# Kernel tuning notes

Measured on AMD Instinct MI355X. Metric: run time of the kernel, lower is better.

Reference implementation:

```python
import jax, jax.numpy as jnp
import numpy as np

B, C, H, W = 8, 256, 96, 96
NQ, NCLS = 100, 12
OBJ_CH = NCLS - 2 + 1  # 11
EPS = 1e-6


def conv2d(x, w, b, pad):
    out = jax.lax.conv_general_dilated(x, w, (1, 1), [(pad, pad), (pad, pad)],
                                       dimension_numbers=('NCHW', 'OIHW', 'NCHW'))
    return out + b[None, :, None, None]


def conv1d(x, w, b):
    out = jax.lax.conv_general_dilated(x, w, (1,), [(0, 0)],
                                       dimension_numbers=('NCH', 'OIH', 'NCH'))
    return out + b[None, :, None]


def adaptive_avg_pool_1d(x, out_size):
    # x: [..., L]; torch AdaptiveAvgPool semantics: bin i = mean(x[floor(i*L/o):ceil((i+1)*L/o)])
    L = x.shape[-1]
    i = np.arange(out_size)
    starts = (i * L) // out_size
    ends = -((-(i + 1) * L) // out_size)
    csum = jnp.concatenate([jnp.zeros(x.shape[:-1] + (1,), x.dtype), jnp.cumsum(x, -1)], -1)
    sizes = jnp.asarray((ends - starts).astype(np.float32))
    return (csum[..., ends] - csum[..., starts]) / sizes


def local_max(p):
    # 8-neighbor local maximum with zero padding, thresholded at EPS
    pd = jnp.pad(p, ((0, 0), (0, 0), (1, 1), (1, 1)))
    m = ((p >= pd[:, :, :-2, 1:-1]) & (p >= pd[:, :, 2:, 1:-1]) &
         (p >= pd[:, :, 1:-1, :-2]) & (p >= pd[:, :, 1:-1, 2:]) &
         (p >= pd[:, :, :-2, :-2]) & (p >= pd[:, :, :-2, 2:]) &
         (p >= pd[:, :, 2:, :-2]) & (p >= pd[:, :, 2:, 2:]) & (p >= EPS))
    return m.astype(p.dtype)


def mask_and_nms(probs):
    # one-hot mask from argmax over foreground channels, then add local-max map
    oh = jax.nn.one_hot(jnp.argmax(probs[:, :-1], axis=1), probs.shape[1], axis=1, dtype=probs.dtype)
    p = probs * oh
    return p + local_max(p)


def head(x, w1, b1, w2, b2):
    return conv2d(jax.nn.relu(conv2d(x, w1, b1, 1)), w2, b2, 0)


def setup_inputs() -> dict:
    key = jax.random.key(0)
    ks = jax.random.split(key, 20)
    rn = lambda k, s: jax.random.normal(k, s, jnp.float32) * 0.02
    z = lambda n: jnp.zeros((n,), jnp.float32)
    return {
        'x': jax.random.normal(ks[0], (B, C, H, W), jnp.float32),
        'y': jax.random.normal(ks[1], (B, C, H, W), jnp.float32),
        'pos_embeddings': jax.random.normal(ks[2], (1, C, H, W), jnp.float32),
        'lw1': rn(ks[3], (C, C, 3, 3)), 'lb1': z(C),
        'lw2': rn(ks[4], (2, C, 1, 1)), 'lb2': z(2),
        'rw1': rn(ks[5], (C, C, 3, 3)), 'rb1': z(C),
        'rw2': rn(ks[6], (2, C, 1, 1)), 'rb2': z(2),
        'ow1': rn(ks[7], (C, C, 3, 3)), 'ob1': z(C),
        'ow2': rn(ks[8], (OBJ_CH, C, 1, 1)), 'ob2': z(OBJ_CH),
        'cw1': rn(ks[9], (64, C, 3, 3)), 'cb1': z(64),
        'cw2': rn(ks[10], (32, 64, 3, 3)), 'cb2': z(32),
        'cm_lw': rn(ks[11], (778 * 2, 778 * 32)), 'cm_lb': z(778 * 2),
        'c1d_w': rn(ks[12], (C, 2, 3)), 'c1d_b': z(C),
        'q_lw': rn(ks[13], (NQ * C, C)), 'q_lb': z(NQ * C),
    }


def reference(x, y, pos_embeddings, lw1, lb1, lw2, lb2, rw1, rb1, rw2, rb2,
              ow1, ob1, ow2, ob2, cw1, cb1, cw2, cb2, cm_lw, cm_lb,
              c1d_w, c1d_b, q_lw, q_lb):
    b = x.shape[0]
    left_logits = head(x, lw1, lb1, lw2, lb2)
    right_logits = head(x, rw1, rb1, rw2, rb2)
    obj_logits = head(x, ow1, ob1, ow2, ob2)

    left_p = mask_and_nms(jax.nn.softmax(left_logits, axis=1))
    right_p = mask_and_nms(jax.nn.softmax(right_logits, axis=1))
    obj_p = mask_and_nms(jax.nn.softmax(obj_logits, axis=1))

    hw = H * W
    idx_l = jax.lax.top_k(left_p[:, 0].reshape(b, hw), 40)[1]
    idx_r = jax.lax.top_k(right_p[:, 0].reshape(b, hw), 40)[1]
    idx_o = jax.lax.top_k(obj_p[:, :-1].reshape(b, OBJ_CH - 1, hw).max(axis=1), 20)[1]
    idx = jnp.concatenate([idx_l, idx_r, idx_o], axis=1)  # [B, 100]

    xf = x.reshape(b, C, hw)
    topk_proposals = jnp.take_along_axis(xf, jnp.broadcast_to(idx[:, None, :], (b, C, NQ)), axis=2)
    pf = jnp.broadcast_to(pos_embeddings, (b, C, H, W)).reshape(b, C, hw)
    topk_pos = jnp.take_along_axis(pf, jnp.broadcast_to(idx[:, None, :], (b, C, NQ)), axis=2)

    # contact map estimation branch
    h = jax.nn.relu(conv2d(y, cw1, cb1, 1))
    h = jax.nn.relu(conv2d(h, cw2, cb2, 1))  # [B,32,H,W]
    h = jnp.mean(h, axis=3)                  # adaptive pool width -> 1
    h = adaptive_avg_pool_1d(h, 778)         # [B,32,778]
    cm = h.reshape(b, -1) @ cm_lw.T + cm_lb  # [B,1556]
    contact_map = cm.reshape(b, 2, 778, 1)

    # ContactMapConvolution
    cc = conv1d(contact_map.reshape(b, 2, 778), c1d_w, c1d_b)  # [B,C,776]
    cc = jnp.mean(cc, axis=2)                                  # [B,C]
    feat = (cc @ q_lw.T + q_lb).reshape(b, C, NQ)              # [B,C,100]

    topk_proposals = topk_proposals + feat
    return (topk_proposals, topk_pos, left_logits, right_logits, obj_logits, contact_map)
```

## Files before the change

kernel.cpp:

```cpp
#include <hip/hip_runtime.h>
#include <float.h>
#include <math.h>

#define B_ 8
#define C_ 256
#define H_ 96
#define W_ 96
#define HW_ 9216
#define NQ_ 100
#define EPS_ 1e-6f
#define PADW_ 98
#define PADIMG_ 9604
#define PALLOC_ 76880

typedef unsigned short ushort_t;
typedef __attribute__((ext_vector_type(8))) short bf16x8;
typedef __attribute__((ext_vector_type(16))) float f32x16;

typedef __attribute__((address_space(3))) unsigned int as3_u32;
typedef __attribute__((address_space(1))) unsigned int as1_u32;

__device__ __forceinline__ void gl16(const void* g, void* l) {
    __builtin_amdgcn_global_load_lds(
        (const as1_u32*)(unsigned long long)g,
        (as3_u32*)(unsigned int)(unsigned long long)l, 16, 0, 0);
}

__device__ __forceinline__ ushort_t bf16_of(float v) {
    unsigned u = __float_as_uint(v);
    u += 0x7fffu + ((u >> 16) & 1u);
    return (ushort_t)(u >> 16);
}
__device__ __forceinline__ float f_of_bf16(ushort_t h) {
    return __uint_as_float((unsigned)h << 16);
}

__global__ __launch_bounds__(256)
void zero_border_kernel(ushort_t* __restrict__ bh, ushort_t* __restrict__ bl, int Cch)
{
    int per = 388 * Cch / 8;
    int id = blockIdx.x * 256 + threadIdx.x;
    if (id >= 8 * per) return;
    int b = id / per, i = id - b * per;
    int pi = (i * 8) / Cch, c8 = (i * 8) % Cch;
    int yy, xx;
    if (pi < 98)      { yy = 0;            xx = pi; }
    else if (pi < 196){ yy = 97;           xx = pi - 98; }
    else if (pi < 292){ yy = pi - 195;     xx = 0; }
    else              { yy = pi - 291;     xx = 97; }
    size_t base = ((size_t)b * PADIMG_ + yy * PADW_ + xx) * Cch + c8;
    *(bf16x8*)&bh[base] = (bf16x8)(short)0;
    *(bf16x8*)&bl[base] = (bf16x8)(short)0;
}

__global__ __launch_bounds__(256)
void tsplit_kernel(const float* __restrict__ in, ushort_t* __restrict__ oh,
                   ushort_t* __restrict__ ol, int Cch)
{
    __shared__ float T[32][33];
    const int tx = threadIdx.x & 31, ty = threadIdx.x >> 5;
    const int p0 = blockIdx.x * 32, ci0 = blockIdx.y * 32, b = blockIdx.z;
#pragma unroll
    for (int i = 0; i < 4; ++i)
        T[ty + 8*i][tx] = in[((size_t)b*Cch + ci0 + ty + 8*i)*HW_ + p0 + tx];
    __syncthreads();
    const int y = p0 / 96, x0 = p0 - y * 96;
    const size_t Pp = (size_t)b*PADIMG_ + (size_t)(y + 1)*PADW_ + x0 + 1;
#pragma unroll
    for (int i = 0; i < 4; ++i) {
        float v = T[tx][ty + 8*i];
        ushort_t hi = bf16_of(v);
        float lo = v - f_of_bf16(hi);
        size_t o = (Pp + ty + 8*i)*Cch + ci0 + tx;
        oh[o] = hi;
        ol[o] = bf16_of(lo);
    }
}

__global__ __launch_bounds__(256)
void repack_kernel(const float* __restrict__ w, ushort_t* __restrict__ wh,
                   ushort_t* __restrict__ wl, int Cout, int Cin)
{
    int id = blockIdx.x*256 + threadIdx.x;
    int tot = 9*Cout*Cin;
    if (id >= tot) return;
    int tap = id / (Cout*Cin);
    int r   = id - tap*(Cout*Cin);
    int g   = r / (Cout*16);
    int r2  = r - g*(Cout*16);
    int oc  = r2 >> 4, cr = r2 & 15;
    int ci  = g*16 + cr;
    float v = w[((size_t)oc*Cin + ci)*9 + tap];
    ushort_t hi = bf16_of(v);
    wh[id] = hi;
    wl[id] = bf16_of(v - f_of_bf16(hi));
}

__global__ __launch_bounds__(256)
void pack_heads3_kernel(const float* lb1, const float* rb1, const float* ob1,
                        const float* lw2, const float* rw2, const float* ow2,
                        const float* lb2, const float* rb2, const float* ob2,
                        float* __restrict__ bias1all, float* __restrict__ w2all,
                        float* __restrict__ b2all)
{
    int i = blockIdx.x * 256 + threadIdx.x;
    if (i < 768) bias1all[i] = (i < 256) ? lb1[i] : (i < 512) ? rb1[i-256] : ob1[i-512];
    if (i < 33) {
        int h = i / 11, k = i - h*11;
        b2all[i] = (h == 0) ? (k < 2 ? lb2[k] : 0.f)
                 : (h == 1) ? (k < 2 ? rb2[k] : 0.f)
                 : ob2[k];
    }
    if (i < 3*11*256) {
        int h = i / 2816, r = i - h*2816;
        int k = r / 256, oc = r - k*256;
        float v = 0.f;
        if (h == 0)      { if (k < 2) v = lw2[k*256 + oc]; }
        else if (h == 1) { if (k < 2) v = rw2[k*256 + oc]; }
        else             v = ow2[k*256 + oc];
        w2all[i] = v;
    }
}

template<int WM, int WN, int MFR, int NFR, int CIN, int MODE>
__global__ __launch_bounds__(WM*WN*64, (WM*WN + 3) / 4)
void conv_gemm_kernel(const ushort_t* __restrict__ Agh, const ushort_t* __restrict__ Agl,
                      const ushort_t* __restrict__ Wgh, const ushort_t* __restrict__ Wgl,
                      const float* __restrict__ bias1,
                      ushort_t* __restrict__ Oth, ushort_t* __restrict__ Otl,
                      float* __restrict__ outf)
{
    constexpr int NW    = WM*WN;
    constexpr int NT    = NW*64;
    constexpr int BM    = WM*MFR*32;
    constexpr int COUT  = WN*NFR*32;
    constexpr int NG    = CIN/16;
    constexpr int APAD  = 512;
    constexpr int ASZ   = 2*APAD*16;
    constexpr int AROUNDS = 32;
    static_assert(BM == 288, "BM must be 288");

    __shared__ __align__(16) ushort_t ALds[2*ASZ];

    const int tid  = threadIdx.x;
    const int lane = tid & 63;
    const int wid  = __builtin_amdgcn_readfirstlane(tid >> 6);
    const int wm   = wid / WN, wn = wid % WN;
    const int l31  = lane & 31, hh2 = lane >> 5;
    const int wnb  = wn * NFR * 32;

    const int cpx = gridDim.x >> 3;
    const int bid = (blockIdx.x & 7)*cpx + (blockIdx.x >> 3);
    const int bidx = bid >> 5;
    const int br   = bid & 31;
    const size_t S = (size_t)bidx*PADIMG_ + (size_t)(3*br)*PADW_;

    auto stageA = [&](int g, int sel) {
        ushort_t* dst = ALds + sel*ASZ;
#pragma unroll 1
        for (int c = wid; c < AROUNDS; c += NW) {
            int id = c*64 + lane;
            int split = id >> 10;
            int r2 = id & 1023;
            int row = r2 >> 1, slot = r2 & 1;
            int ch = slot ^ ((row >> 2) & 1);
            const ushort_t* src = (split ? Agl : Agh) + (S + row)*CIN + g*16 + ch*8;
            gl16(src, dst + (size_t)c*512);
        }
    };

    f32x16 acc[MFR][NFR];
#pragma unroll
    for (int i = 0; i < MFR; ++i)
#pragma unroll
        for (int j = 0; j < NFR; ++j)
#pragma unroll
            for (int r = 0; r < 16; ++r) acc[i][j][r] = 0.f;

    bf16x8 bh0[NFR], bl0[NFR], bh1[NFR], bl1[NFR], bh2[NFR], bl2[NFR];

#define LOADB(G, T, BH, BL)                                                    \
    {                                                                          \
        _Pragma("unroll")                                                      \
        for (int nf = 0; nf < NFR; ++nf) {                                     \
            size_t o = ((size_t)((T)*NG + (G))*COUT + (wnb + nf*32 + l31))*16  \
                       + hh2*8;                                                \
            BH[nf] = *(const bf16x8*)&Wgh[o];                                  \
            BL[nf] = *(const bf16x8*)&Wgl[o];                                  \
        }                                                                      \
    }

    stageA(0, 0);
    LOADB(0, 0, bh0, bl0);
    LOADB(0, 1, bh1, bl1);
    __builtin_amdgcn_sched_barrier(0);
    asm volatile("s_waitcnt vmcnt(%0)" :: "n"(4*NFR) : "memory");
    __builtin_amdgcn_s_barrier();
    __builtin_amdgcn_sched_barrier(0);

#define TAPBODY(T, BHC, BLC, BHN, BLN)                                         \
    {                                                                          \
        if ((T) <= 6)            LOADB(g,     (T)+2, BHN, BLN)                 \
        else if (g + 1 < NG)     LOADB(g+1,   (T)-7, BHN, BLN)                 \
        const int tapoff = ((T)/3)*PADW_ + ((T) % 3);                          \
        _Pragma("unroll")                                                      \
        for (int mf = 0; mf < MFR; ++mf) {                                     \
            int row = wm*PADW_ + tapoff + mf*32 + l31;                         \
            int o = abase + row*16 + ((hh2 ^ ((row >> 2) & 1)) << 3);          \
            bf16x8 ah = *(const bf16x8*)&ALds[o];                              \
            bf16x8 al = *(const bf16x8*)&ALds[o + APAD*16];                    \
            _Pragma("unroll")                                                  \
            for (int nf = 0; nf < NFR; ++nf) {                                 \
                acc[mf][nf] = __builtin_amdgcn_mfma_f32_32x32x16_bf16(         \
                    ah, BHC[nf], acc[mf][nf], 0, 0, 0);                        \
                acc[mf][nf] = __builtin_amdgcn_mfma_f32_32x32x16_bf16(         \
                    al, BHC[nf], acc[mf][nf], 0, 0, 0);                        \
                acc[mf][nf] = __builtin_amdgcn_mfma_f32_32x32x16_bf16(         \
                    ah, BLC[nf], acc[mf][nf], 0, 0, 0);                        \
            }                                                                  \
        }                                                                      \
    }

#pragma unroll 1
    for (int g = 0; g < NG; ++g) {
        if (g + 1 < NG) stageA(g + 1, (g + 1) & 1);
        const int abase = (g & 1) * ASZ;
        TAPBODY(0, bh0, bl0, bh2, bl2);
        TAPBODY(1, bh1, bl1, bh0, bl0);
        TAPBODY(2, bh2, bl2, bh1, bl1);
        TAPBODY(3, bh0, bl0, bh2, bl2);
        TAPBODY(4, bh1, bl1, bh0, bl0);
        TAPBODY(5, bh2, bl2, bh1, bl1);
        TAPBODY(6, bh0, bl0, bh2, bl2);
        TAPBODY(7, bh1, bl1, bh0, bl0);
        TAPBODY(8, bh2, bl2, bh1, bl1);
        __builtin_amdgcn_sched_barrier(0);
        asm volatile("s_waitcnt lgkmcnt(0)" ::: "memory");
        asm volatile("s_waitcnt vmcnt(%0)" :: "n"(4*NFR) : "memory");
        __builtin_amdgcn_s_barrier();
        __builtin_amdgcn_sched_barrier(0);
    }
#undef TAPBODY
#undef LOADB
    __syncthreads();

    float biasv[NFR];
#pragma unroll
    for (int nf = 0; nf < NFR; ++nf) biasv[nf] = bias1[wnb + nf*32 + l31];

    if constexpr (MODE == 1) {
#pragma unroll
        for (int mf = 0; mf < MFR; ++mf)
#pragma unroll
            for (int nf = 0; nf < NFR; ++nf)
#pragma unroll
                for (int r = 0; r < 16; ++r) {
                    float rr = fmaxf(acc[mf][nf][r] + biasv[nf], 0.f);
                    ushort_t hi = bf16_of(rr);
                    float lo = rr - f_of_bf16(hi);
                    int crow = (r & 3) + 8*(r >> 2) + 4*hh2;
                    int xx = mf*32 + crow;
                    size_t Pp = (size_t)bidx*PADIMG_
                              + (size_t)(3*br + wm + 1)*PADW_ + xx + 1;
                    size_t o = Pp*COUT + wnb + nf*32 + l31;
                    Oth[o] = hi;
                    Otl[o] = bf16_of(lo);
                }
    } else {
        float (*T)[BM + 1] = (float(*)[BM + 1])ALds;
#pragma unroll
        for (int mf = 0; mf < MFR; ++mf)
#pragma unroll
            for (int r = 0; r < 16; ++r) {
                float rr = fmaxf(acc[mf][0][r] + biasv[0], 0.f);
                int crow = (r & 3) + 8*(r >> 2) + 4*hh2;
                T[l31][wm*96 + mf*32 + crow] = rr;
            }
        __syncthreads();
        for (int i = tid; i < COUT*BM; i += NT) {
            int c = i / BM, m = i - c*BM;
            outf[((size_t)bidx*COUT + c)*HW_ + br*288 + m] = T[c][m];
        }
    }
}

__global__ __launch_bounds__(256, 3)
void conv_sbu_kernel(const ushort_t* __restrict__ Agh, const ushort_t* __restrict__ Agl,
                     const ushort_t* __restrict__ wLh, const ushort_t* __restrict__ wLl,
                     const ushort_t* __restrict__ wRh, const ushort_t* __restrict__ wRl,
                     const ushort_t* __restrict__ wOh, const ushort_t* __restrict__ wOl,
                     const float* __restrict__ bias1all, const float* __restrict__ w2all,
                     const float* __restrict__ b2all, float* __restrict__ out_logits)
{
    constexpr int NG = 16, APAD = 304, ASZ = 2*APAD*16, AGR = 19, MFR = 3, NFR = 2;
    __shared__ __align__(16) ushort_t ALds[ASZ];

    const int tid  = threadIdx.x;
    const int lane = tid & 63;
    const int wid  = __builtin_amdgcn_readfirstlane(tid >> 6);
    const int l31  = lane & 31, hh2 = lane >> 5;
    const int wnb  = wid * 64;

    const int cpx = gridDim.x >> 3;
    const int bid = (blockIdx.x & 7)*cpx + (blockIdx.x >> 3);
    const int h    = bid / 768;
    const int sub  = bid - h*768;
    const int bidx = sub / 96, prow = sub - bidx*96;
    const int pimg0 = prow * 96;
    const size_t S = (size_t)bidx*PADIMG_ + (size_t)prow*PADW_;

    const ushort_t* Wh = (h == 0) ? wLh : (h == 1) ? wRh : wOh;
    const ushort_t* Wl = (h == 0) ? wLl : (h == 1) ? wRl : wOl;
    const float* bias1 = bias1all + h*256;
    const float* w2    = w2all + (size_t)h*2816;
    const float* b2    = b2all + h*11;
    const int kklim = (h == 2) ? 11 : 2;
    float* dst = out_logits + ((h == 0) ? 0 : (h == 1) ? 147456 : 294912);

    auto stageA = [&](int g) {
#pragma unroll 1
        for (int c = wid; c < AGR; c += 4) {
            int id = c*64 + lane;
            int split = id / (2*APAD);
            int r2 = id % (2*APAD);
            int row = r2 >> 1, slot = r2 & 1;
            int ch = slot ^ ((row >> 2) & 1);
            const ushort_t* src = (split ? Agl : Agh) + (S + row)*C_ + g*16 + ch*8;
            gl16(src, ALds + (size_t)c*512);
        }
    };

    f32x16 acc[MFR][NFR];
#pragma unroll
    for (int i = 0; i < MFR; ++i)
#pragma unroll
        for (int j = 0; j < NFR; ++j)
#pragma unroll
            for (int r = 0; r < 16; ++r) acc[i][j][r] = 0.f;

    bf16x8 bh0[NFR], bl0[NFR], bh1[NFR], bl1[NFR], bh2[NFR], bl2[NFR];

#define LOADB(G, T, BH, BL)                                                    \
    {                                                                          \
        _Pragma("unroll")                                                      \
        for (int nf = 0; nf < NFR; ++nf) {                                     \
            size_t o = ((size_t)((T)*NG + (G))*256 + (wnb + nf*32 + l31))*16   \
                       + hh2*8;                                                \
            BH[nf] = *(const bf16x8*)&Wh[o];                                   \
            BL[nf] = *(const bf16x8*)&Wl[o];                                   \
        }                                                                      \
    }

#define TAPBODY(G, T, BHC, BLC, BHN, BLN)                                      \
    {                                                                          \
        if ((T) <= 6)            LOADB((G), (T)+2, BHN, BLN)                   \
        else if ((G) + 1 < NG)   LOADB((G)+1, (T)-7, BHN, BLN)                 \
        const int tapoff = ((T)/3)*PADW_ + ((T) % 3);                          \
        _Pragma("unroll")                                                      \
        for (int mf = 0; mf < MFR; ++mf) {                                     \
            int row = tapoff + mf*32 + l31;                                    \
            int o = row*16 + ((hh2 ^ ((row >> 2) & 1)) << 3);                  \
            bf16x8 ah = *(const bf16x8*)&ALds[o];                              \
            bf16x8 al = *(const bf16x8*)&ALds[o + APAD*16];                    \
            _Pragma("unroll")                                                  \
            for (int nf = 0; nf < NFR; ++nf) {                                 \
                acc[mf][nf] = __builtin_amdgcn_mfma_f32_32x32x16_bf16(         \
                    ah, BHC[nf], acc[mf][nf], 0, 0, 0);                        \
                acc[mf][nf] = __builtin_amdgcn_mfma_f32_32x32x16_bf16(         \
                    al, BHC[nf], acc[mf][nf], 0, 0, 0);                        \
                acc[mf][nf] = __builtin_amdgcn_mfma_f32_32x32x16_bf16(         \
                    ah, BLC[nf], acc[mf][nf], 0, 0, 0);                        \
            }                                                                  \
        }                                                                      \
    }

#define STAGEWAIT(G)                                                           \
    __builtin_amdgcn_sched_barrier(0);                                         \
    asm volatile("s_waitcnt lgkmcnt(0)" ::: "memory");                         \
    __builtin_amdgcn_sched_barrier(0);                                         \
    __builtin_amdgcn_s_barrier();             \
    stageA(G);                                                                 \
    __builtin_amdgcn_sched_barrier(0);                                         \
    asm volatile("s_waitcnt vmcnt(0)" ::: "memory");                           \
    __builtin_amdgcn_s_barrier();                                              \
    __builtin_amdgcn_sched_barrier(0);

    LOADB(0, 0, bh0, bl0);
    LOADB(0, 1, bh1, bl1);

#pragma unroll 1
    for (int g = 0; g < NG; ++g) {
        STAGEWAIT(g)
        TAPBODY(g, 0, bh0, bl0, bh2, bl2);
        TAPBODY(g, 1, bh1, bl1, bh0, bl0);
        TAPBODY(g, 2, bh2, bl2, bh1, bl1);
        TAPBODY(g, 3, bh0, bl0, bh2, bl2);
        TAPBODY(g, 4, bh1, bl1, bh0, bl0);
        TAPBODY(g, 5, bh2, bl2, bh1, bl1);
        TAPBODY(g, 6, bh0, bl0, bh2, bl2);
        TAPBODY(g, 7, bh1, bl1, bh0, bl0);
        TAPBODY(g, 8, bh2, bl2, bh1, bl1);
    }
#undef STAGEWAIT
#undef TAPBODY
#undef LOADB
    __syncthreads();

    float biasv[NFR];
#pragma unroll
    for (int nf = 0; nf < NFR; ++nf) biasv[nf] = bias1[wnb + nf*32 + l31];
    float w2v[NFR][11];
#pragma unroll
    for (int nf = 0; nf < NFR; ++nf)
#pragma unroll
        for (int k = 0; k < 11; ++k) w2v[nf][k] = w2[k*256 + wnb + nf*32 + l31];

    float* Lacc = (float*)ALds;
#pragma unroll
    for (int mf = 0; mf < MFR; ++mf) {
#pragma unroll
        for (int r = 0; r < 16; ++r) {
            float v[11];
#pragma unroll
            for (int k = 0; k < 11; ++k) v[k] = 0.f;
#pragma unroll
            for (int nf = 0; nf < NFR; ++nf) {
                float rr = fmaxf(acc[mf][nf][r] + biasv[nf], 0.f);
#pragma unroll
                for (int k = 0; k < 11; ++k)
                    if (k < kklim) v[k] += rr * w2v[nf][k];
            }
#pragma unroll
            for (int k = 0; k < 11; ++k) {
                if (k < kklim) {
                    v[k] += __shfl_xor(v[k], 1);
                    v[k] += __shfl_xor(v[k], 2);
                    v[k] += __shfl_xor(v[k], 4);
                    v[k] += __shfl_xor(v[k], 8);
                    v[k] += __shfl_xor(v[k], 16);
                }
            }
            if (l31 == 0) {
                int crow = (r & 3) + 8*(r >> 2) + 4*hh2;
                int row96 = mf*32 + crow;
#pragma unroll
                for (int k = 0; k < 11; ++k)
                    if (k < kklim)
                        Lacc[((size_t)wid*96 + row96)*11 + k] = v[k];
            }
        }
    }
    __syncthreads();
    for (int i = tid; i < 96*kklim; i += 256) {
        int row96 = i / kklim, k = i - row96*kklim;
        float s = b2[k];
#pragma unroll
        for (int w = 0; w < 4; ++w) s += Lacc[((size_t)w*96 + row96)*11 + k];
        dst[((size_t)bidx*kklim + k)*HW_ + pimg0 + row96] = s;
    }
}

__global__ __launch_bounds__(256)
void prob2b_kernel(const float* __restrict__ l2, const float* __restrict__ l3,
                   float* __restrict__ pL, float* __restrict__ pR)
{
    const float* logits = blockIdx.y ? l3 : l2;
    float* p0 = blockIdx.y ? pR : pL;
    int i = blockIdx.x * 256 + threadIdx.x;
    if (i >= B_ * HW_) return;
    int b = i / HW_, pix = i - b * HW_;
    float l0 = logits[(size_t)b * 2 * HW_ + pix];
    float l1 = logits[(size_t)b * 2 * HW_ + HW_ + pix];
    float m = fmaxf(l0, l1);
    float e0 = expf(l0 - m), e1 = expf(l1 - m);
    p0[i] = e0 / (e0 + e1);
}

__global__ __launch_bounds__(256)
void score2b_kernel(const float* __restrict__ pL, const float* __restrict__ pR,
                    float* __restrict__ sL, float* __restrict__ sR)
{
    const float* p = blockIdx.y ? pR : pL;
    float* sc = blockIdx.y ? sR : sL;
    int i = blockIdx.x * 256 + threadIdx.x;
    if (i >= B_ * HW_) return;
    int pix = i % HW_;
    int yy = pix / W_, xx = pix - (pix / W_) * W_;
    float c = p[i];
    bool ok = (c >= EPS_);
    const float* pb = p + (i - pix);
#pragma unroll
    for (int dy = -1; dy <= 1; ++dy)
#pragma unroll
        for (int dx = -1; dx <= 1; ++dx) {
            if (dy == 0 && dx == 0) continue;
            int ny = yy + dy, nx = xx + dx;
            float v = 0.f;
            if (ny >= 0 && ny < H_ && nx >= 0 && nx < W_) v = pb[ny * W_ + nx];
            ok = ok && (c >= v);
        }
    sc[i] = c + (ok ? 1.f : 0.f);
}

__global__ __launch_bounds__(256)
void probobj_kernel(const float* __restrict__ logits, float* __restrict__ pval,
                    int* __restrict__ cstar)
{
    int i = blockIdx.x * 256 + threadIdx.x;
    if (i >= B_ * HW_) return;
    int b = i / HW_, pix = i - b * HW_;
    const float* lb = logits + (size_t)b * 11 * HW_ + pix;
    float l[11];
#pragma unroll
    for (int c2 = 0; c2 < 11; ++c2) l[c2] = lb[(size_t)c2 * HW_];
    float m = l[0];
#pragma unroll
    for (int c2 = 1; c2 < 11; ++c2) m = fmaxf(m, l[c2]);
    float sum = 0.f;
#pragma unroll
    for (int c2 = 0; c2 < 11; ++c2) sum += expf(l[c2] - m);
    int a = 0; float bestl = l[0];
#pragma unroll
    for (int c2 = 1; c2 < 10; ++c2)
        if (l[c2] > bestl) { bestl = l[c2]; a = c2; }
    pval[i] = expf(bestl - m) / sum;
    cstar[i] = a;
}

__global__ __launch_bounds__(256)
void score11_kernel(const float* __restrict__ p, const int* __restrict__ cs,
                    float* __restrict__ sc)
{
    int i = blockIdx.x * 256 + threadIdx.x;
    if (i >= B_ * HW_) return;
    int pix = i % HW_;
    int yy = pix / W_, xx = pix - (pix / W_) * W_;
    float c = p[i];
    int cc = cs[i];
    bool ok = (c >= EPS_);
    int base = i - pix;
#pragma unroll
    for (int dy = -1; dy <= 1; ++dy)
#pragma unroll
        for (int dx = -1; dx <= 1; ++dx) {
            if (dy == 0 && dx == 0) continue;
            int ny = yy + dy, nx = xx + dx;
            float v = 0.f;
            if (ny >= 0 && ny < H_ && nx >= 0 && nx < W_) {
                int n = base + ny * W_ + nx;
                v = (cs[n] == cc) ? p[n] : 0.f;
            }
            ok = ok && (c >= v);
        }
    sc[i] = c + (ok ? 1.f : 0.f);
}

__global__ __launch_bounds__(256)
void topk_kernel(const float* __restrict__ scL, const float* __restrict__ scR,
                 const float* __restrict__ scO, int* __restrict__ idx)
{
    __shared__ float sv[HW_];
    __shared__ float rv[256];
    __shared__ int   ri[256];
    const int h = blockIdx.x, b = blockIdx.y;
    const float* src = (h == 0) ? scL : (h == 1) ? scR : scO;
    const int k = (h == 2) ? 20 : 40;
    const int off = b * NQ_ + ((h == 0) ? 0 : (h == 1) ? 40 : 80);

    for (int t = threadIdx.x; t < HW_; t += 256) sv[t] = src[(size_t)b * HW_ + t];
    __syncthreads();

    for (int kk = 0; kk < k; ++kk) {
        float bestv = -FLT_MAX; int besti = HW_;
        for (int t = threadIdx.x; t < HW_; t += 256) {
            float v = sv[t];
            if (v > bestv) { bestv = v; besti = t; }
        }
        rv[threadIdx.x] = bestv; ri[threadIdx.x] = besti;
        __syncthreads();
        for (int s = 128; s > 0; s >>= 1) {
            if (threadIdx.x < s) {
                float v2 = rv[threadIdx.x + s]; int i2 = ri[threadIdx.x + s];
                if (v2 > rv[threadIdx.x] ||
                    (v2 == rv[threadIdx.x] && i2 < ri[threadIdx.x])) {
                    rv[threadIdx.x] = v2; ri[threadIdx.x] = i2;
                }
            }
            __syncthreads();
        }
        if (threadIdx.x == 0) { idx[off + kk] = ri[0]; sv[ri[0]] = -FLT_MAX; }
        __syncthreads();
    }
}

__global__ __launch_bounds__(128)
void pool_kernel(const float* __restrict__ h2, float* __restrict__ pooled)
{
    int bc = blockIdx.x;
    __shared__ float row[96];
    for (int hh = threadIdx.x; hh < 96; hh += 128) {
        const float* p = h2 + (size_t)bc * HW_ + hh * W_;
        float s = 0.f;
        for (int ww = 0; ww < 96; ++ww) s += p[ww];
        row[hh] = s * (1.f / 96.f);
    }
    __syncthreads();
    for (int i = threadIdx.x; i < 778; i += 128) {
        int s0 = (i * 96) / 778;
        int e0 = ((i + 1) * 96 + 777) / 778;
        float s = 0.f;
        for (int t = s0; t < e0; ++t) s += row[t];
        pooled[(size_t)bc * 778 + i] = s / (float)(e0 - s0);
    }
}

__global__ __launch_bounds__(256)
void cm_kernel(const float* __restrict__ pooled, const float* __restrict__ cm_lw,
               const float* __restrict__ cm_lb, float* __restrict__ out5)
{
    const int j = blockIdx.x;
    const float* wr = cm_lw + (size_t)j * 24896;
    float acc[8];
#pragma unroll
    for (int b = 0; b < 8; ++b) acc[b] = 0.f;
    for (int t = threadIdx.x; t < 24896; t += 256) {
        float w = wr[t];
#pragma unroll
        for (int b = 0; b < 8; ++b) acc[b] += w * pooled[(size_t)b * 24896 + t];
    }
    __shared__ float red[8][256];
#pragma unroll
    for (int b = 0; b < 8; ++b) red[b][threadIdx.x] = acc[b];
    __syncthreads();
    for (int s = 128; s > 0; s >>= 1) {
        if (threadIdx.x < s) {
#pragma unroll
            for (int b = 0; b < 8; ++b) red[b][threadIdx.x] += red[b][threadIdx.x + s];
        }
        __syncthreads();
    }
    if (threadIdx.x < 8)
        out5[(size_t)threadIdx.x * 1556 + j] = red[threadIdx.x][0] + cm_lb[j];
}

__global__ __launch_bounds__(256)
void c1d_kernel(const float* __restrict__ cmap, const float* __restrict__ w,
                const float* __restrict__ bias, float* __restrict__ ccmean)
{
    int b = blockIdx.x;
    __shared__ float r[2][778];
    __shared__ float T[2][3];
    for (int t = threadIdx.x; t < 1556; t += 256)
        r[t / 778][t % 778] = cmap[(size_t)b * 1556 + t];
    __syncthreads();
    if (threadIdx.x < 2) {
        int ic = threadIdx.x;
        float s = 0.f;
        for (int i2 = 0; i2 < 778; ++i2) s += r[ic][i2];
        T[ic][0] = s - r[ic][776] - r[ic][777];
        T[ic][1] = s - r[ic][0]   - r[ic][777];
        T[ic][2] = s - r[ic][0]   - r[ic][1];
    }
    __syncthreads();
    int oc = threadIdx.x;
    float a = 0.f;
#pragma unroll
    for (int ic = 0; ic < 2; ++ic)
#pragma unroll
        for (int k = 0; k < 3; ++k)
            a += w[oc * 6 + ic * 3 + k] * T[ic][k];
    ccmean[b * 256 + oc] = a / 776.f + bias[oc];
}

__global__ __launch_bounds__(256)
void feat_kernel(const float* __restrict__ ccmean, const float* __restrict__ q_lw,
                 const float* __restrict__ q_lb, float* __restrict__ feat)
{
    __shared__ float cc[8][256];
    for (int t = threadIdx.x; t < 2048; t += 256) cc[t >> 8][t & 255] = ccmean[t];
    __syncthreads();
    int j = blockIdx.x * 256 + threadIdx.x;
    const float* wr = q_lw + (size_t)j * 256;
    float acc[8];
#pragma unroll
    for (int b = 0; b < 8; ++b) acc[b] = 0.f;
    for (int c = 0; c < 256; ++c) {
        float wv = wr[c];
#pragma unroll
        for (int b = 0; b < 8; ++b) acc[b] += wv * cc[b][c];
    }
    float qb = q_lb[j];
#pragma unroll
    for (int b = 0; b < 8; ++b) feat[(size_t)b * 25600 + j] = acc[b] + qb;
}

__global__ __launch_bounds__(256)
void gather_kernel(const float* __restrict__ x, const float* __restrict__ pos,
                   const float* __restrict__ feat, const int* __restrict__ idx,
                   float* __restrict__ out0, float* __restrict__ out1)
{
    int t = blockIdx.x * 256 + threadIdx.x;
    if (t >= B_ * C_ * NQ_) return;
    int q = t % NQ_;
    int c2 = (t / NQ_) % C_;
    int b = t / (C_ * NQ_);
    int p = idx[b * NQ_ + q];
    out0[t] = x[((size_t)b * C_ + c2) * HW_ + p] + feat[(size_t)b * 25600 + c2 * NQ_ + q];
    out1[t] = pos[(size_t)c2 * HW_ + p];
}

extern "C" void kernel_launch(void* const* d_in, const int* in_sizes, int n_in,
                              void* d_out, int out_size, void* d_ws, size_t ws_size,
                              hipStream_t stream) {
    const float* x    = (const float*)d_in[0];
    const float* y    = (const float*)d_in[1];
    const float* pos  = (const float*)d_in[2];
    const float* lw1  = (const float*)d_in[3];  const float* lb1 = (const float*)d_in[4];
    const float* lw2  = (const float*)d_in[5];  const float* lb2 = (const float*)d_in[6];
    const float* rw1  = (const float*)d_in[7];  const float* rb1 = (const float*)d_in[8];
    const float* rw2  = (const float*)d_in[9];  const float* rb2 = (const float*)d_in[10];
    const float* ow1  = (const float*)d_in[11]; const float* ob1 = (const float*)d_in[12];
    const float* ow2  = (const float*)d_in[13]; const float* ob2 = (const float*)d_in[14];
    const float* cw1  = (const float*)d_in[15]; const float* cb1 = (const float*)d_in[16];
    const float* cw2  = (const float*)d_in[17]; const float* cb2 = (const float*)d_in[18];
    const float* cmlw = (const float*)d_in[19]; const float* cmlb = (const float*)d_in[20];
    const float* c1dw = (const float*)d_in[21]; const float* c1db = (const float*)d_in[22];
    const float* qlw  = (const float*)d_in[23]; const float* qlb  = (const float*)d_in[24];

    float* out  = (float*)d_out;
    float* out0 = out;
    float* out1 = out + 204800;
    float* out2 = out + 409600;
    float* out3 = out + 557056;
    float* out4 = out + 704512;
    float* out5 = out + 1515520;

    float* ws = (float*)d_ws;
    ushort_t* Rh   = (ushort_t*)(ws);
    ushort_t* Rl   = (ushort_t*)(ws + 9840640);
    ushort_t* h1h  = (ushort_t*)(ws + 19681280);
    ushort_t* h1l  = (ushort_t*)(ws + 22141440);
    float*    h2   = ws + 24601600;
    ushort_t* wLh  = (ushort_t*)(ws + 26960896);
    ushort_t* wLl  = (ushort_t*)(ws + 27255808);
    ushort_t* wRh  = (ushort_t*)(ws + 27550720);
    ushort_t* wRl  = (ushort_t*)(ws + 27845632);
    ushort_t* wOh  = (ushort_t*)(ws + 28140544);
    ushort_t* wOl  = (ushort_t*)(ws + 28435456);
    ushort_t* wc1h = (ushort_t*)(ws + 28730368);
    ushort_t* wc1l = (ushort_t*)(ws + 28804096);
    ushort_t* wc2h = (ushort_t*)(ws + 28877824);
    ushort_t* wc2l = (ushort_t*)(ws + 28887040);
    float* pooled  = ws + 28896256;
    float* ccmean  = ws + 29095424;
    float* feat    = ws + 29097472;
    float* pmapL   = ws + 29302272;
    int*   csmap   = (int*)(ws + 29376000);
    float* scL     = ws + 29449728;
    float* scR     = ws + 29523456;
    float* scO     = ws + 29597184;
    int*   idxb    = (int*)(ws + 29670912);
    float* bias1all= ws + 29671712;
    float* w2all   = ws + 29672480;
    float* b2all   = ws + 29680928;
    float* pmapR   = ws + 29680976;
    float* pmapO   = ws + 29754704;
    (void)in_sizes; (void)n_in; (void)out_size; (void)ws_size; (void)pos;

    zero_border_kernel<<<388, 256, 0, stream>>>(Rh, Rl, 256);
    zero_border_kernel<<<97,  256, 0, stream>>>(h1h, h1l, 64);
    repack_kernel<<<(9*256*256+255)/256, 256, 0, stream>>>(lw1, wLh, wLl, 256, 256);
    repack_kernel<<<(9*256*256+255)/256, 256, 0, stream>>>(rw1, wRh, wRl, 256, 256);
    repack_kernel<<<(9*256*256+255)/256, 256, 0, stream>>>(ow1, wOh, wOl, 256, 256);
    repack_kernel<<<(9*64*256+255)/256,  256, 0, stream>>>(cw1, wc1h, wc1l, 64, 256);
    repack_kernel<<<(9*32*64+255)/256,   256, 0, stream>>>(cw2, wc2h, wc2l, 32, 64);
    pack_heads3_kernel<<<33, 256, 0, stream>>>(lb1, rb1, ob1, lw2, rw2, ow2,
                                               lb2, rb2, ob2, bias1all, w2all, b2all);

    tsplit_kernel<<<dim3(288, 8, 8), 256, 0, stream>>>(y, Rh, Rl, 256);
    conv_gemm_kernel<3,2,3,1,256,1><<<256, 384, 0, stream>>>(
        Rh, Rl, wc1h, wc1l, cb1, h1h, h1l, nullptr);
    conv_gemm_kernel<3,1,3,1,64,2><<<256, 192, 0, stream>>>(
        h1h, h1l, wc2h, wc2l, cb2, nullptr, nullptr, h2);
    pool_kernel<<<256, 128, 0, stream>>>(h2, pooled);
    cm_kernel<<<1556, 256, 0, stream>>>(pooled, cmlw, cmlb, out5);
    c1d_kernel<<<8, 256, 0, stream>>>(out5, c1dw, c1db, ccmean);
    feat_kernel<<<100, 256, 0, stream>>>(ccmean, qlw, qlb, feat);

    tsplit_kernel<<<dim3(288, 8, 8), 256, 0, stream>>>(x, Rh, Rl, 256);
    conv_sbu_kernel<<<2304, 256, 0, stream>>>(
        Rh, Rl, wLh, wLl, wRh, wRl, wOh, wOl, bias1all, w2all, b2all, out2);

    prob2b_kernel<<<dim3(288, 2), 256, 0, stream>>>(out2, out3, pmapL, pmapR);
    score2b_kernel<<<dim3(288, 2), 256, 0, stream>>>(pmapL, pmapR, scL, scR);
    probobj_kernel<<<288, 256, 0, stream>>>(out4, pmapO, csmap);
    score11_kernel<<<288, 256, 0, stream>>>(pmapO, csmap, scO);

    topk_kernel<<<dim3(3, 8), 256, 0, stream>>>(scL, scR, scO, idxb);
    gather_kernel<<<800, 256, 0, stream>>>(x, pos, feat, idxb, out0, out1);
}
```

Baseline: 1.323 ms.

## Reduce weight prefetch depth to two buffers and remap block-to-row order

The weight-fragment prefetch in the conv head kernel drops from three register buffers (two taps ahead) to two buffers (one tap ahead). The group loop is unrolled by two so buffer roles alternate correctly across odd and even group counts. This frees VGPRs, which may help hold occupancy, but leaves less latency hiding for the global weight loads. The block-to-work mapping also changes: each head now gets a contiguous block range, and within it batches are interleaved by row instead of heads being spread across the grid.

Result: faster. 1.239 ms (-6.4%).

```diff
diff --git a/kernel.cpp b/kernel.cpp
--- a/kernel.cpp
+++ b/kernel.cpp
@@ -301,10 +301,9 @@
     const int l31  = lane & 31, hh2 = lane >> 5;
     const int wnb  = wid * 64;
 
-    const int cpx = gridDim.x >> 3;
-    const int bid = (blockIdx.x & 7)*cpx + (blockIdx.x >> 3);
-    const int h    = bid / 768;
-    const int sub  = bid - h*768;
+    const int h    = blockIdx.x / 768;
+    const int subx = blockIdx.x - h*768;
+    const int sub  = (subx & 7)*96 + (subx >> 3);
     const int bidx = sub / 96, prow = sub - bidx*96;
     const int pimg0 = prow * 96;
     const size_t S = (size_t)bidx*PADIMG_ + (size_t)prow*PADW_;
@@ -338,7 +337,7 @@
 #pragma unroll
             for (int r = 0; r < 16; ++r) acc[i][j][r] = 0.f;
 
-    bf16x8 bh0[NFR], bl0[NFR], bh1[NFR], bl1[NFR], bh2[NFR], bl2[NFR];
+    bf16x8 bhX[NFR], blX[NFR], bhY[NFR], blY[NFR];
 
 #define LOADB(G, T, BH, BL)                                                    \
     {                                                                          \
@@ -353,8 +352,8 @@
 
 #define TAPBODY(G, T, BHC, BLC, BHN, BLN)                                      \
     {                                                                          \
-        if ((T) <= 6)            LOADB((G), (T)+2, BHN, BLN)                   \
-        else if ((G) + 1 < NG)   LOADB((G)+1, (T)-7, BHN, BLN)                 \
+        if ((T) < 8)             LOADB((G), (T)+1, BHN, BLN)                   \
+        else if ((G) + 1 < NG)   LOADB((G)+1, 0, BHN, BLN)                     \
         const int tapoff = ((T)/3)*PADW_ + ((T) % 3);                          \
         _Pragma("unroll")                                                      \
         for (int mf = 0; mf < MFR; ++mf) {                                     \
@@ -374,6 +373,19 @@
         }                                                                      \
     }
 
+#define GROUPBODY(G, S0h, S0l, S1h, S1l)                                       \
+    {                                                                          \
+        TAPBODY((G), 0, S0h, S0l, S1h, S1l);                                   \
+        TAPBODY((G), 1, S1h, S1l, S0h, S0l);                                   \
+        TAPBODY((G), 2, S0h, S0l, S1h, S1l);                                   \
+        TAPBODY((G), 3, S1h, S1l, S0h, S0l);                                   \
+        TAPBODY((G), 4, S0h, S0l, S1h, S1l);                                   \
+        TAPBODY((G), 5, S1h, S1l, S0h, S0l);                                   \
+        TAPBODY((G), 6, S0h, S0l, S1h, S1l);                                   \
+        TAPBODY((G), 7, S1h, S1l, S0h, S0l);                                   \
+        TAPBODY((G), 8, S0h, S0l, S1h, S1l);                                   \
+    }
+
 #define STAGEWAIT(G)                                                           \
     __builtin_amdgcn_sched_barrier(0);                                         \
     asm volatile("s_waitcnt lgkmcnt(0)" ::: "memory");                         \
@@ -385,23 +397,17 @@
     __builtin_amdgcn_s_barrier();                                              \
     __builtin_amdgcn_sched_barrier(0);
 
-    LOADB(0, 0, bh0, bl0);
-    LOADB(0, 1, bh1, bl1);
+    LOADB(0, 0, bhX, blX);
 
 #pragma unroll 1
-    for (int g = 0; g < NG; ++g) {
+    for (int g = 0; g < NG; g += 2) {
         STAGEWAIT(g)
-        TAPBODY(g, 0, bh0, bl0, bh2, bl2);
-        TAPBODY(g, 1, bh1, bl1, bh0, bl0);
-        TAPBODY(g, 2, bh2, bl2, bh1, bl1);
-        TAPBODY(g, 3, bh0, bl0, bh2, bl2);
-        TAPBODY(g, 4, bh1, bl1, bh0, bl0);
-        TAPBODY(g, 5, bh2, bl2, bh1, bl1);
-        TAPBODY(g, 6, bh0, bl0, bh2, bl2);
-        TAPBODY(g, 7, bh1, bl1, bh0, bl0);
-        TAPBODY(g, 8, bh2, bl2, bh1, bl1);
+        GROUPBODY(g,     bhX, blX, bhY, blY);
+        STAGEWAIT(g + 1)
+        GROUPBODY(g + 1, bhY, blY, bhX, blX);
     }
 #undef STAGEWAIT
+#undef GROUPBODY
 #undef TAPBODY
 #undef LOADB
     __syncthreads();
```
